# Kernel tuning notes

Hardware: AMD Instinct MI355X
Metric: run time of the kernel (lower is better)

## Reference

```python
import jax, jax.numpy as jnp
import numpy as np

K = 5  # k_neighbors


def _pairwise_sq(a, b):
    # (B,N,3),(B,M,3) -> (B,N,M) squared euclidean distances (matmul form)
    d = (jnp.sum(a * a, -1)[:, :, None] + jnp.sum(b * b, -1)[:, None, :]
         - 2.0 * jnp.einsum('bnd,bmd->bnm', a, b))
    return jnp.maximum(d, 0.0)


def _knn_indices(points, k):
    # (B,N,3) -> (B,N,k) indices of k nearest neighbors, excluding self
    d = _pairwise_sq(points, points)
    _, idx = jax.lax.top_k(-d, k + 1)
    return idx[:, :, 1:]


def _gather_neighbors(feats, idx):
    # feats (B,N,C), idx (B,N,k) -> (B,N,k,C)
    B, N, k = idx.shape
    flat = jnp.take_along_axis(feats, idx.reshape(B, N * k, 1), axis=1)
    return flat.reshape(B, N, k, feats.shape[-1])


def setup_inputs() -> dict:
    key = jax.random.key(0)
    ks = jax.random.split(key, 8)
    B, N, M = 8, 4096, 4000
    return {
        'Y': jax.random.normal(ks[0], (B, N, 3), jnp.float32),
        'X': jax.random.normal(ks[1], (B, M, 3), jnp.float32),
        'R_pred': jax.random.normal(ks[2], (B, 3, 3), jnp.float32),
        't_pred': jax.random.normal(ks[3], (B, 3), jnp.float32),
        'R_gt': jax.random.normal(ks[4], (B, 3, 3), jnp.float32),
        't_gt': jax.random.normal(ks[5], (B, 3), jnp.float32),
        'X_hat': jax.random.normal(ks[6], (B, N, 3), jnp.float32),
        'delta': jax.random.normal(ks[7], (B, N, 3), jnp.float32),
    }


def reference(Y, X, R_pred, t_pred, R_gt, t_gt, X_hat, delta):
    lam_rot, lam_trans, lam_rmse = 1.0, 1.0, 1.0
    lam_align, lam_disp, lam_deform, lam_lap = 1.0, 0.01, 0.1, 0.1

    # --- rigid losses ---
    # rotation geodesic: R_delta = R_pred^T @ R_gt
    R_delta = jnp.einsum('bij,bik->bjk', R_pred, R_gt)
    tr = jnp.trace(R_delta, axis1=1, axis2=2)
    cos_a = jnp.clip((tr - 1.0) / 2.0, -1.0 + 1e-7, 1.0 - 1e-7)
    L_rot = jnp.mean(jnp.arccos(cos_a))

    L_trans = jnp.mean(jnp.linalg.norm(t_pred - t_gt, axis=1))

    # Y @ R^T + t
    Y_pred = jnp.einsum('bnd,bkd->bnk', Y, R_pred) + t_pred[:, None, :]
    Y_gt = jnp.einsum('bnd,bkd->bnk', Y, R_gt) + t_gt[:, None, :]
    L_rmse = jnp.mean(jnp.sqrt(jnp.mean(jnp.sum((Y_pred - Y_gt) ** 2, -1), axis=1)))

    rigid = lam_rot * L_rot + lam_trans * L_trans + lam_rmse * L_rmse

    # --- non-rigid losses ---
    Y_rigid = Y_pred  # apply_rigid_transform(Y, R_pred, t_pred)

    # alignment: N != M -> kNN matching of X_hat against X
    d_align = _pairwise_sq(X_hat, X)          # (B,N,M)
    knn_d = -jax.lax.top_k(-d_align, K)[0]    # (B,N,K) smallest distances
    L_align = jnp.mean(knn_d)

    L_disp = jnp.mean(jnp.sum(delta ** 2, -1))

    # kNN graph on Y_rigid (original builds it twice with identical result)
    idx = _knn_indices(Y_rigid, K)            # (B,N,K)

    Yn = _gather_neighbors(Y_rigid, idx)      # (B,N,K,3)
    Xn = _gather_neighbors(X_hat, idx)
    edge_diff = (Xn - X_hat[:, :, None, :]) - (Yn - Y_rigid[:, :, None, :])
    L_deform = jnp.mean(jnp.sum(edge_diff ** 2, -1))

    dn = _gather_neighbors(delta, idx)        # (B,N,K,3)
    lap = delta - jnp.mean(dn, axis=2)
    L_lap = jnp.mean(jnp.sum(lap ** 2, -1))

    non_rigid = (lam_align * L_align + lam_disp * L_disp
                 + lam_deform * L_deform + lam_lap * L_lap)
    total = rigid + non_rigid

    return jnp.stack([total, rigid, non_rigid, L_rot, L_trans, L_rmse,
                      L_align, L_disp, L_deform, L_lap])
```

## Files before the change

### kernel.cpp

```cpp
#include <hip/hip_runtime.h>
#include <math.h>

#define BB 8
#define NN 4096
#define MM 4000
#define KK 5
#define NWAVE 8
#define QG 128
#define CH 256
#define HSZ 2048
#define NPAD 4096
#define MQ_BLK 256
#define M_BLOCKS (BB * NN / MQ_BLK)

#define ACC_ROT    0
#define ACC_TRANS  1
#define ACC_ALIGN  2
#define ACC_DISP   3
#define ACC_DEFORM 4
#define ACC_LAP    5
#define ACC_RMSE   6
#define ACC_COUNT  14

#define INFF __int_as_float(0x7F800000)

__device__ __forceinline__ float waveReduceSum(float v) {
#pragma unroll
    for (int off = 32; off > 0; off >>= 1) v += __shfl_down(v, off, 64);
    return v;
}

template<bool SELF, bool PACK>
__device__ __forceinline__ void proc1(float4 c, int midx, int q,
                                      float ca, float cbq, float cc,
                                      float& b0, float& b1, float& b2,
                                      float& b3, float& b4) {
    float sc = fmaf(c.x, ca, fmaf(c.y, cbq, fmaf(c.z, cc, c.w)));
    float v;
    if (PACK) {
        unsigned pk = (__float_as_uint(sc) & 0xFFFFF000u) | (unsigned)midx;
        v = __uint_as_float(pk);
        if (SELF) v = (midx == q) ? INFF : v;
    } else {
        v = sc;
    }
    float n0 = fminf(b0, v);
    float n1 = __builtin_amdgcn_fmed3f(v, b0, b1);
    float n2 = __builtin_amdgcn_fmed3f(v, b1, b2);
    float n3 = __builtin_amdgcn_fmed3f(v, b2, b3);
    float n4 = __builtin_amdgcn_fmed3f(v, b3, b4);
    b0 = n0; b1 = n1; b2 = n2; b3 = n3; b4 = n4;
}

template<bool SELF, bool PACK>
__device__ __forceinline__ void scanLDS2(const float4* lc, int tl, int tg,
                                         float a0, float b0c, float c0, int q0,
                                         float a1, float b1c, float c1, int q1,
                                         float& x0, float& x1, float& x2,
                                         float& x3, float& x4,
                                         float& y0, float& y1, float& y2,
                                         float& y3, float& y4) {
    float4 A[4], B[4];
#pragma unroll
    for (int j = 0; j < 4; ++j) A[j] = lc[tl + j];

    for (int t0 = 0; t0 < CH; t0 += 8) {
#pragma unroll
        for (int j = 0; j < 4; ++j) B[j] = lc[tl + t0 + 4 + j];
#pragma unroll
        for (int j = 0; j < 4; ++j) {
            proc1<SELF, PACK>(A[j], tg + t0 + j, q0, a0, b0c, c0, x0, x1, x2, x3, x4);
            proc1<SELF, PACK>(A[j], tg + t0 + j, q1, a1, b1c, c1, y0, y1, y2, y3, y4);
        }
        if (t0 + 8 < CH) {
#pragma unroll
            for (int j = 0; j < 4; ++j) A[j] = lc[tl + t0 + 8 + j];
        }
#pragma unroll
        for (int j = 0; j < 4; ++j) {
            proc1<SELF, PACK>(B[j], tg + t0 + 4 + j, q0, a0, b0c, c0, x0, x1, x2, x3, x4);
            proc1<SELF, PACK>(B[j], tg + t0 + 4 + j, q1, a1, b1c, c1, y0, y1, y2, y3, y4);
        }
    }
}

__global__ void k_prep(const float* __restrict__ Y, const float* __restrict__ X,
                       const float* __restrict__ Rp, const float* __restrict__ tp,
                       const float* __restrict__ Rg, const float* __restrict__ tg,
                       const float* __restrict__ dl,
                       float4* __restrict__ YrP, float4* __restrict__ XP,
                       float* __restrict__ acc) {
    int b = blockIdx.x >> 4;
    int n = ((blockIdx.x & 15) << 8) + threadIdx.x;
    size_t base = ((size_t)b * NN + n) * 3;
    float yx = Y[base + 0], yy = Y[base + 1], yz = Y[base + 2];

    float rp[9], rg[9], tpv[3], tgv[3];
#pragma unroll
    for (int i = 0; i < 9; ++i) { rp[i] = Rp[b * 9 + i]; rg[i] = Rg[b * 9 + i]; }
#pragma unroll
    for (int i = 0; i < 3; ++i) { tpv[i] = tp[b * 3 + i]; tgv[i] = tg[b * 3 + i]; }

    float p[3], dr2 = 0.f;
#pragma unroll
    for (int k = 0; k < 3; ++k) {
        float pv = fmaf(yx, rp[k * 3 + 0], fmaf(yy, rp[k * 3 + 1], fmaf(yz, rp[k * 3 + 2], tpv[k])));
        float gv = fmaf(yx, rg[k * 3 + 0], fmaf(yy, rg[k * 3 + 1], fmaf(yz, rg[k * 3 + 2], tgv[k])));
        p[k] = pv;
        float dd = pv - gv;
        dr2 = fmaf(dd, dd, dr2);
    }
    YrP[(size_t)b * NPAD + n] =
        make_float4(p[0], p[1], p[2], fmaf(p[0], p[0], fmaf(p[1], p[1], p[2] * p[2])));

    float4 xe;
    if (n < MM) {
        size_t xb = ((size_t)b * MM + n) * 3;
        float x0 = X[xb + 0], x1 = X[xb + 1], x2 = X[xb + 2];
        xe = make_float4(x0, x1, x2, fmaf(x0, x0, fmaf(x1, x1, x2 * x2)));
    } else {
        xe = make_float4(0.f, 0.f, 0.f, INFF);
    }
    XP[(size_t)b * NPAD + n] = xe;

    float d0 = dl[base + 0], d1 = dl[base + 1], d2 = dl[base + 2];
    float dsq = d0 * d0 + d1 * d1 + d2 * d2;

    dr2 = waveReduceSum(dr2);
    dsq = waveReduceSum(dsq);
    if ((threadIdx.x & 63) == 0) {
        atomicAdd(&acc[ACC_RMSE + b], dr2);
        atomicAdd(&acc[ACC_DISP], dsq);
    }

    if (threadIdx.x == 0 && (blockIdx.x & 15) == 0) {
        float tr = 0.f;
#pragma unroll
        for (int i = 0; i < 9; ++i) tr += rp[i] * rg[i];
        float c = (tr - 1.f) * 0.5f;
        c = fminf(fmaxf(c, -1.f + 1e-7f), 1.f - 1e-7f);
        float dx = tpv[0] - tgv[0], dy = tpv[1] - tgv[1], dz = tpv[2] - tgv[2];
        atomicAdd(&acc[ACC_ROT], acosf(c));
        atomicAdd(&acc[ACC_TRANS], sqrtf(dx * dx + dy * dy + dz * dz));
    }
}

#define MERGE_STEP(W) { float d = mdp[((W) * QG + l) * 6 + pp##W]; if (d < best) { best = d; bw = W; } }
#define MERGE_ADV()  { pp0 += (bw == 0); pp1 += (bw == 1); pp2 += (bw == 2); pp3 += (bw == 3); \
                       pp4 += (bw == 4); pp5 += (bw == 5); pp6 += (bw == 6); pp7 += (bw == 7); }

__global__ __launch_bounds__(512, 6) void k_scan(const float* __restrict__ Xh,
                                                 const float4* __restrict__ XP,
                                                 const float4* __restrict__ YrP,
                                                 float* __restrict__ pa,
                                                 float* __restrict__ pk) {
    __shared__ float4 lsbuf[HSZ];
    float* mdp = (float*)lsbuf;
    int tid = threadIdx.x, wave = tid >> 6, lane = tid & 63;
    int qg = blockIdx.x, b = blockIdx.y;
    int half = blockIdx.z & 1, mode = blockIdx.z >> 1;
    int q0 = qg * QG + lane, q1 = q0 + 64;

    const float4* cbG = (mode == 0 ? XP : YrP) + (size_t)b * NPAD;
#pragma unroll
    for (int i = 0; i < HSZ / 512; ++i)
        lsbuf[tid + i * 512] = cbG[half * HSZ + tid + i * 512];

    float qx0, qy0, qz0, qx1, qy1, qz1;
    if (mode == 0) {
        size_t a0 = ((size_t)b * NN + q0) * 3;
        size_t a1 = ((size_t)b * NN + q1) * 3;
        qx0 = Xh[a0 + 0]; qy0 = Xh[a0 + 1]; qz0 = Xh[a0 + 2];
        qx1 = Xh[a1 + 0]; qy1 = Xh[a1 + 1]; qz1 = Xh[a1 + 2];
    } else {
        float4 p0 = cbG[q0], p1 = cbG[q1];
        qx0 = p0.x; qy0 = p0.y; qz0 = p0.z;
        qx1 = p1.x; qy1 = p1.y; qz1 = p1.z;
    }
    __syncthreads();

    float x0 = INFF, x1 = INFF, x2 = INFF, x3 = INFF, x4 = INFF;
    float y0 = INFF, y1 = INFF, y2 = INFF, y3 = INFF, y4 = INFF;
    int tl = wave * CH;
    int tg = half * HSZ + tl;
    bool hasSelf = (mode == 1) && (half == (qg >> 4)) && (wave == ((qg >> 1) & 7));
    if (mode == 0) {
        scanLDS2<false, false>(lsbuf, tl, tg,
                               -2.f * qx0, -2.f * qy0, -2.f * qz0, 0,
                               -2.f * qx1, -2.f * qy1, -2.f * qz1, 0,
                               x0, x1, x2, x3, x4, y0, y1, y2, y3, y4);
    } else if (hasSelf) {
        scanLDS2<true, true>(lsbuf, tl, tg,
                             -2.f * qx0, -2.f * qy0, -2.f * qz0, q0,
                             -2.f * qx1, -2.f * qy1, -2.f * qz1, q1,
                             x0, x1, x2, x3, x4, y0, y1, y2, y3, y4);
    } else {
        scanLDS2<false, true>(lsbuf, tl, tg,
                              -2.f * qx0, -2.f * qy0, -2.f * qz0, q0,
                              -2.f * qx1, -2.f * qy1, -2.f * qz1, q1,
                              x0, x1, x2, x3, x4, y0, y1, y2, y3, y4);
    }
    __syncthreads();

    float* m0 = &mdp[(wave * QG + lane) * 6];
    m0[0] = x0; m0[1] = x1; m0[2] = x2; m0[3] = x3; m0[4] = x4; m0[5] = INFF;
    float* m1 = &mdp[(wave * QG + lane + 64) * 6];
    m1[0] = y0; m1[1] = y1; m1[2] = y2; m1[3] = y3; m1[4] = y4; m1[5] = INFF;
    __syncthreads();

    if (tid < QG) {
        int l = tid;
        int q = qg * QG + l;
        int pp0 = 0, pp1 = 0, pp2 = 0, pp3 = 0, pp4 = 0, pp5 = 0, pp6 = 0, pp7 = 0;
        float* dst = (mode == 0 ? pa : pk) + (((size_t)b * NN + q) * 2 + half) * 6;
#pragma unroll
        for (int k = 0; k < KK; ++k) {
            float best = INFF; int bw = 0;
            MERGE_STEP(0) MERGE_STEP(1) MERGE_STEP(2) MERGE_STEP(3)
            MERGE_STEP(4) MERGE_STEP(5) MERGE_STEP(6) MERGE_STEP(7)
            dst[k] = best;
            MERGE_ADV()
        }
        dst[5] = INFF;
    }
}

__device__ void finalize(const float* acc, float* out) {
    float a[ACC_COUNT];
#pragma unroll
    for (int i = 0; i < ACC_COUNT; ++i)
        a[i] = __hip_atomic_load(&acc[i], __ATOMIC_RELAXED, __HIP_MEMORY_SCOPE_AGENT);
    float L_rot = a[ACC_ROT] / BB;
    float L_trans = a[ACC_TRANS] / BB;
    float L_rmse = 0.f;
#pragma unroll
    for (int b = 0; b < BB; ++b) L_rmse += sqrtf(a[ACC_RMSE + b] / NN);
    L_rmse /= BB;
    float L_align = a[ACC_ALIGN] / ((float)BB * NN * KK);
    float L_disp = a[ACC_DISP] / ((float)BB * NN);
    float L_def = a[ACC_DEFORM] / ((float)BB * NN * KK);
    float L_lap = a[ACC_LAP] / ((float)BB * NN);
    float rigid = L_rot + L_trans + L_rmse;
    float nr = L_align + 0.01f * L_disp + 0.1f * L_def + 0.1f * L_lap;
    out[0] = rigid + nr; out[1] = rigid; out[2] = nr;
    out[3] = L_rot; out[4] = L_trans; out[5] = L_rmse;
    out[6] = L_align; out[7] = L_disp; out[8] = L_def; out[9] = L_lap;
}

__global__ void k_merge(const float4* __restrict__ YrP, const float* __restrict__ Xh,
                        const float* __restrict__ dl, const float* __restrict__ pa,
                        const float* __restrict__ pk, float* __restrict__ acc,
                        unsigned* __restrict__ doneCnt, float* __restrict__ out) {
    int gid = blockIdx.x * MQ_BLK + threadIdx.x;
    int b = gid >> 12, q = gid & (NN - 1);

    size_t qb = (size_t)gid * 3;
    float qhx = Xh[qb + 0], qhy = Xh[qb + 1], qhz = Xh[qb + 2];
    float qn = fmaf(qhx, qhx, fmaf(qhy, qhy, qhz * qhz));
    {
        const float* p0 = pa + (size_t)gid * 12;
        const float* p1 = p0 + 6;
        int i = 0, j = 0;
        float s = 0.f;
#pragma unroll
        for (int k = 0; k < KK; ++k) {
            float a = p0[i], c = p1[j];
            bool ta = (a <= c);
            s += fmaxf((ta ? a : c) + qn, 0.f);
            i += ta; j += !ta;
        }
        s = waveReduceSum(s);
        if ((threadIdx.x & 63) == 0) atomicAdd(&acc[ACC_ALIGN], s);
    }

    const float4* cb = YrP + (size_t)b * NPAD;
    float4 qp = cb[q];
    const float* p0 = pk + (size_t)gid * 12;
    const float* p1 = p0 + 6;
    int i = 0, j = 0;
    int si[KK];
#pragma unroll
    for (int k = 0; k < KK; ++k) {
        float a = p0[i], c = p1[j];
        bool ta = (a <= c);
        si[k] = (int)(__float_as_uint(ta ? a : c) & 0xFFFu);
        i += ta; j += !ta;
    }

    const float* xh = Xh + (size_t)b * NN * 3;
    const float* dlb = dl + (size_t)b * NN * 3;
    float xnx = xh[q * 3 + 0], xny = xh[q * 3 + 1], xnz = xh[q * 3 + 2];
    float dnx = dlb[q * 3 + 0], dny = dlb[q * 3 + 1], dnz = dlb[q * 3 + 2];

    float def = 0.f, sx = 0.f, sy = 0.f, sz = 0.f;
#pragma unroll
    for (int k = 0; k < KK; ++k) {
        int n = si[k];
        float4 yj = cb[n];
        float ex = (xh[n * 3 + 0] - xnx) - (yj.x - qp.x);
        float ey = (xh[n * 3 + 1] - xny) - (yj.y - qp.y);
        float ez = (xh[n * 3 + 2] - xnz) - (yj.z - qp.z);
        def += ex * ex + ey * ey + ez * ez;
        sx += dlb[n * 3 + 0]; sy += dlb[n * 3 + 1]; sz += dlb[n * 3 + 2];
    }
    float lx = dnx - sx / 5.f, ly = dny - sy / 5.f, lz = dnz - sz / 5.f;
    float lap = lx * lx + ly * ly + lz * lz;

    def = waveReduceSum(def);
    lap = waveReduceSum(lap);
    if ((threadIdx.x & 63) == 0) {
        atomicAdd(&acc[ACC_DEFORM], def);
        atomicAdd(&acc[ACC_LAP], lap);
    }
    __syncthreads();
    if (threadIdx.x == 0) {
        __threadfence();
        unsigned t = __hip_atomic_fetch_add(doneCnt, 1u, __ATOMIC_ACQ_REL,
                                            __HIP_MEMORY_SCOPE_AGENT);
        if (t == M_BLOCKS - 1) finalize(acc, out);
    }
}

extern "C" void kernel_launch(void* const* d_in, const int* in_sizes, int n_in,
                              void* d_out, int out_size, void* d_ws, size_t ws_size,
                              hipStream_t stream) {
    const float* Y  = (const float*)d_in[0];
    const float* X  = (const float*)d_in[1];
    const float* Rp = (const float*)d_in[2];
    const float* tp = (const float*)d_in[3];
    const float* Rg = (const float*)d_in[4];
    const float* tg = (const float*)d_in[5];
    const float* Xh = (const float*)d_in[6];
    const float* dl = (const float*)d_in[7];
    float* out = (float*)d_out;

    float*    acc     = (float*)d_ws;
    unsigned* doneCnt = (unsigned*)((char*)d_ws + 64);
    float4*   YrP     = (float4*)((char*)d_ws + 512);
    float4*   XP      = YrP + (size_t)BB * NPAD;
    float*    pa      = (float*)(XP + (size_t)BB * NPAD);
    float*    pk      = pa + (size_t)BB * NN * 12;

    hipMemsetAsync(d_ws, 0, 512, stream);
    hipLaunchKernelGGL(k_prep, dim3(BB * NN / 256), dim3(256), 0, stream,
                       Y, X, Rp, tp, Rg, tg, dl, YrP, XP, acc);
    hipLaunchKernelGGL(k_scan, dim3(NN / QG, BB, 4), dim3(512), 0, stream,
                       Xh, XP, YrP, pa, pk);
    hipLaunchKernelGGL(k_merge, dim3(M_BLOCKS), dim3(MQ_BLK), 0, stream,
                       YrP, Xh, dl, pa, pk, acc, doneCnt, out);
}
```

Baseline: 115.2 us.

## Fuse kNN merge stage into scan kernel via last-arriving-half counter

Removes the separate k_merge launch. Each (mode, batch, query-group) pair of k_scan blocks now bumps a per-group atomic counter after writing its partial top-K lists, and the second block to arrive merges both halves. For mode 0 it accumulates the alignment sum; for mode 1 it gathers neighbours for the deform and Laplacian terms. The last group to finish computes the final outputs. This saves one kernel launch and the dependency gap between kernels, at the cost of extra atomics, a larger workspace memset, and merge work done by only 128 of 512 threads in the arriving block.

```diff
diff --git a/kernel.cpp b/kernel.cpp
--- a/kernel.cpp
+++ b/kernel.cpp
@@ -10,8 +10,7 @@
 #define CH 256
 #define HSZ 2048
 #define NPAD 4096
-#define MQ_BLK 256
-#define M_BLOCKS (BB * NN / MQ_BLK)
+#define NGROUP (32 * BB * 2)
 
 #define ACC_ROT    0
 #define ACC_TRANS  1
@@ -145,6 +144,28 @@
     }
 }
 
+__device__ void finalize(const float* acc, float* out) {
+    float a[ACC_COUNT];
+#pragma unroll
+    for (int i = 0; i < ACC_COUNT; ++i)
+        a[i] = __hip_atomic_load(&acc[i], __ATOMIC_RELAXED, __HIP_MEMORY_SCOPE_AGENT);
+    float L_rot = a[ACC_ROT] / BB;
+    float L_trans = a[ACC_TRANS] / BB;
+    float L_rmse = 0.f;
+#pragma unroll
+    for (int b = 0; b < BB; ++b) L_rmse += sqrtf(a[ACC_RMSE + b] / NN);
+    L_rmse /= BB;
+    float L_align = a[ACC_ALIGN] / ((float)BB * NN * KK);
+    float L_disp = a[ACC_DISP] / ((float)BB * NN);
+    float L_def = a[ACC_DEFORM] / ((float)BB * NN * KK);
+    float L_lap = a[ACC_LAP] / ((float)BB * NN);
+    float rigid = L_rot + L_trans + L_rmse;
+    float nr = L_align + 0.01f * L_disp + 0.1f * L_def + 0.1f * L_lap;
+    out[0] = rigid + nr; out[1] = rigid; out[2] = nr;
+    out[3] = L_rot; out[4] = L_trans; out[5] = L_rmse;
+    out[6] = L_align; out[7] = L_disp; out[8] = L_def; out[9] = L_lap;
+}
+
 #define MERGE_STEP(W) { float d = mdp[((W) * QG + l) * 6 + pp##W]; if (d < best) { best = d; bw = W; } }
 #define MERGE_ADV()  { pp0 += (bw == 0); pp1 += (bw == 1); pp2 += (bw == 2); pp3 += (bw == 3); \
                        pp4 += (bw == 4); pp5 += (bw == 5); pp6 += (bw == 6); pp7 += (bw == 7); }
@@ -152,9 +173,15 @@
 __global__ __launch_bounds__(512, 6) void k_scan(const float* __restrict__ Xh,
                                                  const float4* __restrict__ XP,
                                                  const float4* __restrict__ YrP,
+                                                 const float* __restrict__ dl,
                                                  float* __restrict__ pa,
-                                                 float* __restrict__ pk) {
+                                                 float* __restrict__ pk,
+                                                 float* __restrict__ acc,
+                                                 unsigned* __restrict__ hcnt,
+                                                 unsigned* __restrict__ doneCnt,
+                                                 float* __restrict__ out) {
     __shared__ float4 lsbuf[HSZ];
+    __shared__ unsigned rank;
     float* mdp = (float*)lsbuf;
     int tid = threadIdx.x, wave = tid >> 6, lane = tid & 63;
     int qg = blockIdx.x, b = blockIdx.y;
@@ -223,101 +250,84 @@
         }
         dst[5] = INFF;
     }
-}
-
-__device__ void finalize(const float* acc, float* out) {
-    float a[ACC_COUNT];
-#pragma unroll
-    for (int i = 0; i < ACC_COUNT; ++i)
-        a[i] = __hip_atomic_load(&acc[i], __ATOMIC_RELAXED, __HIP_MEMORY_SCOPE_AGENT);
-    float L_rot = a[ACC_ROT] / BB;
-    float L_trans = a[ACC_TRANS] / BB;
-    float L_rmse = 0.f;
-#pragma unroll
-    for (int b = 0; b < BB; ++b) L_rmse += sqrtf(a[ACC_RMSE + b] / NN);
-    L_rmse /= BB;
-    float L_align = a[ACC_ALIGN] / ((float)BB * NN * KK);
-    float L_disp = a[ACC_DISP] / ((float)BB * NN);
-    float L_def = a[ACC_DEFORM] / ((float)BB * NN * KK);
-    float L_lap = a[ACC_LAP] / ((float)BB * NN);
-    float rigid = L_rot + L_trans + L_rmse;
-    float nr = L_align + 0.01f * L_disp + 0.1f * L_def + 0.1f * L_lap;
-    out[0] = rigid + nr; out[1] = rigid; out[2] = nr;
-    out[3] = L_rot; out[4] = L_trans; out[5] = L_rmse;
-    out[6] = L_align; out[7] = L_disp; out[8] = L_def; out[9] = L_lap;
-}
-
-__global__ void k_merge(const float4* __restrict__ YrP, const float* __restrict__ Xh,
-                        const float* __restrict__ dl, const float* __restrict__ pa,
-                        const float* __restrict__ pk, float* __restrict__ acc,
-                        unsigned* __restrict__ doneCnt, float* __restrict__ out) {
-    int gid = blockIdx.x * MQ_BLK + threadIdx.x;
-    int b = gid >> 12, q = gid & (NN - 1);
-
-    size_t qb = (size_t)gid * 3;
-    float qhx = Xh[qb + 0], qhy = Xh[qb + 1], qhz = Xh[qb + 2];
-    float qn = fmaf(qhx, qhx, fmaf(qhy, qhy, qhz * qhz));
-    {
-        const float* p0 = pa + (size_t)gid * 12;
-        const float* p1 = p0 + 6;
-        int i = 0, j = 0;
-        float s = 0.f;
-#pragma unroll
-        for (int k = 0; k < KK; ++k) {
-            float a = p0[i], c = p1[j];
-            bool ta = (a <= c);
-            s += fmaxf((ta ? a : c) + qn, 0.f);
-            i += ta; j += !ta;
-        }
-        s = waveReduceSum(s);
-        if ((threadIdx.x & 63) == 0) atomicAdd(&acc[ACC_ALIGN], s);
-    }
-
-    const float4* cb = YrP + (size_t)b * NPAD;
-    float4 qp = cb[q];
-    const float* p0 = pk + (size_t)gid * 12;
-    const float* p1 = p0 + 6;
-    int i = 0, j = 0;
-    int si[KK];
-#pragma unroll
-    for (int k = 0; k < KK; ++k) {
-        float a = p0[i], c = p1[j];
-        bool ta = (a <= c);
-        si[k] = (int)(__float_as_uint(ta ? a : c) & 0xFFFu);
-        i += ta; j += !ta;
-    }
-
-    const float* xh = Xh + (size_t)b * NN * 3;
-    const float* dlb = dl + (size_t)b * NN * 3;
-    float xnx = xh[q * 3 + 0], xny = xh[q * 3 + 1], xnz = xh[q * 3 + 2];
-    float dnx = dlb[q * 3 + 0], dny = dlb[q * 3 + 1], dnz = dlb[q * 3 + 2];
-
-    float def = 0.f, sx = 0.f, sy = 0.f, sz = 0.f;
-#pragma unroll
-    for (int k = 0; k < KK; ++k) {
-        int n = si[k];
-        float4 yj = cb[n];
-        float ex = (xh[n * 3 + 0] - xnx) - (yj.x - qp.x);
-        float ey = (xh[n * 3 + 1] - xny) - (yj.y - qp.y);
-        float ez = (xh[n * 3 + 2] - xnz) - (yj.z - qp.z);
-        def += ex * ex + ey * ey + ez * ez;
-        sx += dlb[n * 3 + 0]; sy += dlb[n * 3 + 1]; sz += dlb[n * 3 + 2];
-    }
-    float lx = dnx - sx / 5.f, ly = dny - sy / 5.f, lz = dnz - sz / 5.f;
-    float lap = lx * lx + ly * ly + lz * lz;
-
-    def = waveReduceSum(def);
-    lap = waveReduceSum(lap);
-    if ((threadIdx.x & 63) == 0) {
-        atomicAdd(&acc[ACC_DEFORM], def);
-        atomicAdd(&acc[ACC_LAP], lap);
-    }
-    __syncthreads();
-    if (threadIdx.x == 0) {
+
+    __syncthreads();
+    if (tid == 0) {
+        __threadfence();
+        unsigned gi = ((unsigned)mode * BB + b) * 32 + qg;
+        rank = __hip_atomic_fetch_add(&hcnt[gi], 1u, __ATOMIC_ACQ_REL,
+                                      __HIP_MEMORY_SCOPE_AGENT);
+    }
+    __syncthreads();
+    if (rank == 0) return;
+
+    if (tid < QG) {
+        int l = tid;
+        int q = qg * QG + l;
+        int gid = b * NN + q;
+        if (mode == 0) {
+            size_t a0 = (size_t)gid * 3;
+            float qx = Xh[a0 + 0], qy = Xh[a0 + 1], qz = Xh[a0 + 2];
+            float qn = fmaf(qx, qx, fmaf(qy, qy, qz * qz));
+            const float* p0 = pa + (size_t)gid * 12;
+            const float* p1 = p0 + 6;
+            int i = 0, j = 0;
+            float s = 0.f;
+#pragma unroll
+            for (int k = 0; k < KK; ++k) {
+                float a = p0[i], c = p1[j];
+                bool ta = (a <= c);
+                s += fmaxf((ta ? a : c) + qn, 0.f);
+                i += ta; j += !ta;
+            }
+            s = waveReduceSum(s);
+            if ((l & 63) == 0) atomicAdd(&acc[ACC_ALIGN], s);
+        } else {
+            const float* p0 = pk + (size_t)gid * 12;
+            const float* p1 = p0 + 6;
+            int i = 0, j = 0;
+            int si[KK];
+#pragma unroll
+            for (int k = 0; k < KK; ++k) {
+                float a = p0[i], c = p1[j];
+                bool ta = (a <= c);
+                si[k] = (int)(__float_as_uint(ta ? a : c) & 0xFFFu);
+                i += ta; j += !ta;
+            }
+            float4 qp = cbG[q];
+            const float* xh = Xh + (size_t)b * NN * 3;
+            const float* dlb = dl + (size_t)b * NN * 3;
+            float xnx = xh[q * 3 + 0], xny = xh[q * 3 + 1], xnz = xh[q * 3 + 2];
+            float dnx = dlb[q * 3 + 0], dny = dlb[q * 3 + 1], dnz = dlb[q * 3 + 2];
+
+            float def = 0.f, sx = 0.f, sy = 0.f, sz = 0.f;
+#pragma unroll
+            for (int k = 0; k < KK; ++k) {
+                int n = si[k];
+                float4 yj = cbG[n];
+                float ex = (xh[n * 3 + 0] - xnx) - (yj.x - qp.x);
+                float ey = (xh[n * 3 + 1] - xny) - (yj.y - qp.y);
+                float ez = (xh[n * 3 + 2] - xnz) - (yj.z - qp.z);
+                def += ex * ex + ey * ey + ez * ez;
+                sx += dlb[n * 3 + 0]; sy += dlb[n * 3 + 1]; sz += dlb[n * 3 + 2];
+            }
+            float lx = dnx - sx / 5.f, ly = dny - sy / 5.f, lz = dnz - sz / 5.f;
+            float lap = lx * lx + ly * ly + lz * lz;
+
+            def = waveReduceSum(def);
+            lap = waveReduceSum(lap);
+            if ((l & 63) == 0) {
+                atomicAdd(&acc[ACC_DEFORM], def);
+                atomicAdd(&acc[ACC_LAP], lap);
+            }
+        }
+    }
+    __syncthreads();
+    if (tid == 0) {
         __threadfence();
         unsigned t = __hip_atomic_fetch_add(doneCnt, 1u, __ATOMIC_ACQ_REL,
                                             __HIP_MEMORY_SCOPE_AGENT);
-        if (t == M_BLOCKS - 1) finalize(acc, out);
+        if (t == NGROUP - 1) finalize(acc, out);
     }
 }
 
@@ -334,18 +344,18 @@
     const float* dl = (const float*)d_in[7];
     float* out = (float*)d_out;
 
-    float*    acc     = (float*)d_ws;
-    unsigned* doneCnt = (unsigned*)((char*)d_ws + 64);
-    float4*   YrP     = (float4*)((char*)d_ws + 512);
+    char* w = (char*)d_ws;
+    float*    acc     = (float*)w;
+    unsigned* doneCnt = (unsigned*)(w + 64);
+    unsigned* hcnt    = (unsigned*)(w + 128);
+    float4*   YrP     = (float4*)(w + 4096);
     float4*   XP      = YrP + (size_t)BB * NPAD;
     float*    pa      = (float*)(XP + (size_t)BB * NPAD);
     float*    pk      = pa + (size_t)BB * NN * 12;
 
-    hipMemsetAsync(d_ws, 0, 512, stream);
+    hipMemsetAsync(d_ws, 0, 4096, stream);
     hipLaunchKernelGGL(k_prep, dim3(BB * NN / 256), dim3(256), 0, stream,
                        Y, X, Rp, tp, Rg, tg, dl, YrP, XP, acc);
     hipLaunchKernelGGL(k_scan, dim3(NN / QG, BB, 4), dim3(512), 0, stream,
-                       Xh, XP, YrP, pa, pk);
-    hipLaunchKernelGGL(k_merge, dim3(M_BLOCKS), dim3(MQ_BLK), 0, stream,
-                       YrP, Xh, dl, pa, pk, acc, doneCnt, out);
-}
+                       Xh, XP, YrP, dl, pa, pk, acc, hcnt, doneCnt, out);
+}
```

After: 121.0 us. +5.0%, slower.
